# Optimization experiments

Measured on AMD Instinct MI355X. Metric: run time of the kernel, lower is better.

The kernel has to match this reference:

```python
import jax, jax.numpy as jnp
import numpy as np

NEG_SLOPE = 0.2
EPS = 0.0  # default eps, non-trainable buffer
N_NODES = 50000
N_EDGES = 400000
D = 512  # state_dim


def setup_inputs() -> dict:
    key = jax.random.key(0)
    ks = jax.random.split(key, 8)
    x = jax.random.normal(ks[0], (N_NODES, D), dtype=jnp.float32)
    row = jax.random.randint(ks[1], (N_EDGES,), 0, N_NODES)
    col = jax.random.randint(ks[2], (N_EDGES,), 0, N_NODES)
    # remove_self_loops: guarantee no self loops at data-gen time (static shapes)
    col = jnp.where(row == col, (col + 1) % N_NODES, col)
    edge_index = jnp.stack([row, col], axis=0)  # [2, E]
    condition = jax.random.normal(ks[3], (1, 256), dtype=jnp.float32)
    scale = 1.0 / np.sqrt(256.0)
    Wk = jax.random.normal(ks[4], (256, 2 * D), dtype=jnp.float32) * scale
    W1 = jax.random.normal(ks[5], (D, 2 * D), dtype=jnp.float32) / np.sqrt(D)
    b1 = jnp.zeros((2 * D,), dtype=jnp.float32)
    W2 = jax.random.normal(ks[6], (2 * D, D), dtype=jnp.float32) / np.sqrt(2 * D)
    b2 = jnp.zeros((D,), dtype=jnp.float32)
    return {"x": x, "edge_index": edge_index, "condition": condition,
            "Wk": Wk, "W1": W1, "b1": b1, "W2": W2, "b2": b2}


def reference(x, edge_index, condition, Wk, W1, b1, W2, b2):
    row, col = edge_index[0], edge_index[1]
    key = condition @ Wk                      # [1, 2D]
    ki, kj = key[0, :D], key[0, D:]           # x_i pairs with first half, x_j with second
    x_i = x[col]                              # [E, D]
    # alpha = (cat([x_i, x_j]) * key).sum(-1) without materializing the concat
    alpha = x_i @ ki + x[row] @ kj            # [E]
    alpha = jnp.where(alpha >= 0, alpha, NEG_SLOPE * alpha)  # leaky_relu
    alpha = jax.nn.sigmoid(alpha)
    agg = jax.ops.segment_sum(x_i * alpha[:, None], row, num_segments=x.shape[0])
    out = (1.0 + EPS) * x + agg
    out = jax.nn.relu(out @ W1 + b1) @ W2 + b2  # h_Theta MLP
    return out
```

## Files before the change

kernel.cpp:

```cpp
#include <hip/hip_runtime.h>

#define D 512
#define H1 1024
#define NNODES 50000
#define NEDGES 400000
#define MPAD 50048
#define NEG_SLOPE 0.2f
#define SCAN_BLOCKS 196

typedef __attribute__((ext_vector_type(8))) short bf16x8;
typedef __attribute__((ext_vector_type(8))) unsigned short u16x8;
typedef __attribute__((ext_vector_type(4))) float f32x4;


__device__ __forceinline__ unsigned short f2bf(float f) {
  unsigned int u = __float_as_uint(f);
  unsigned int r = u + 0x7FFFu + ((u >> 16) & 1u);
  return (unsigned short)(r >> 16);
}
__device__ __forceinline__ float bf2f(unsigned short h) {
  return __uint_as_float((unsigned int)h << 16);
}

__device__ __forceinline__ void gl_lds16(const void* g, void* l) {
  __builtin_amdgcn_global_load_lds(
      (const __attribute__((address_space(1))) void*)g,
      (__attribute__((address_space(3))) void*)l, 16, 0, 0);
}

__global__ void key_kernel(const float* __restrict__ cond, const float* __restrict__ Wk,
                           float* __restrict__ key) {
  int j = blockIdx.x * blockDim.x + threadIdx.x;
  if (j >= 2 * D) return;
  float s = 0.f;
#pragma unroll 8
  for (int i = 0; i < 256; ++i) s += cond[i] * Wk[i * (2 * D) + j];
  key[j] = s;
}

__global__ void nodedot_kernel(const float* __restrict__ x, const float* __restrict__ key,
                               float* __restrict__ nki, float* __restrict__ nkj,
                               unsigned short* __restrict__ xb) {
  int wid = (blockIdx.x * blockDim.x + threadIdx.x) >> 6;
  int lane = threadIdx.x & 63;
  if (wid >= NNODES) return;
  const float4* xr = (const float4*)(x + (size_t)wid * D);
  float4 p0 = xr[2 * lane], p1 = xr[2 * lane + 1];
  const float4* kia = (const float4*)key;
  const float4* kja = (const float4*)(key + D);
  float4 q0 = kia[2 * lane], q1 = kia[2 * lane + 1];
  float4 r0 = kja[2 * lane], r1 = kja[2 * lane + 1];
  float a = p0.x * q0.x + p0.y * q0.y + p0.z * q0.z + p0.w * q0.w +
            p1.x * q1.x + p1.y * q1.y + p1.z * q1.z + p1.w * q1.w;
  float b = p0.x * r0.x + p0.y * r0.y + p0.z * r0.z + p0.w * r0.w +
            p1.x * r1.x + p1.y * r1.y + p1.z * r1.z + p1.w * r1.w;
  u16x8 h;
  h[0] = f2bf(p0.x); h[1] = f2bf(p0.y); h[2] = f2bf(p0.z); h[3] = f2bf(p0.w);
  h[4] = f2bf(p1.x); h[5] = f2bf(p1.y); h[6] = f2bf(p1.z); h[7] = f2bf(p1.w);
  *(u16x8*)(xb + (size_t)wid * D + 8 * lane) = h;
#pragma unroll
  for (int off = 32; off > 0; off >>= 1) {
    a += __shfl_xor(a, off);
    b += __shfl_xor(b, off);
  }
  if (lane == 0) { nki[wid] = a; nkj[wid] = b; }
}

__global__ void convw_kernel(const float* __restrict__ W1, const float* __restrict__ W2,
                             unsigned short* __restrict__ W1t, unsigned short* __restrict__ W2t) {
  int idx = blockIdx.x * blockDim.x + threadIdx.x;
  if (idx >= D * H1) return;
  {
    int k = idx / H1, n = idx % H1;
    size_t a = (((size_t)(n >> 7) * (D >> 3) + (k >> 3)) << 10) + ((n & 127) << 3) + (k & 7);
    W1t[a] = f2bf(W1[idx]);
  }
  {
    int k = idx / D, n = idx % D;
    size_t a = (((size_t)(n >> 7) * (H1 >> 3) + (k >> 3)) << 10) + ((n & 127) << 3) + (k & 7);
    W2t[a] = f2bf(W2[idx]);
  }
}

__global__ void zero_deg_kernel(int* __restrict__ deg) {
  int i = blockIdx.x * blockDim.x + threadIdx.x;
  if (i < NNODES) deg[i] = 0;
}

__global__ void hist_kernel(const int* __restrict__ row, int* __restrict__ deg) {
  int e = blockIdx.x * blockDim.x + threadIdx.x;
  if (e < NEDGES) atomicAdd(&deg[row[e]], 1);
}

__global__ void scan1_kernel(const int* __restrict__ deg, int* __restrict__ rowptr,
                             int* __restrict__ blktot) {
  __shared__ int s[256];
  int tid = threadIdx.x;
  int i = blockIdx.x * 256 + tid;
  int v = (i < NNODES) ? deg[i] : 0;
  s[tid] = v;
  __syncthreads();
#pragma unroll
  for (int off = 1; off < 256; off <<= 1) {
    int t = (tid >= off) ? s[tid - off] : 0;
    __syncthreads();
    s[tid] += t;
    __syncthreads();
  }
  if (i < NNODES) rowptr[i] = s[tid] - v;
  if (tid == 255) blktot[blockIdx.x] = s[255];
}

__global__ void scan2_kernel(int* __restrict__ blktot, int* __restrict__ blkoff) {
  __shared__ int s[256];
  int tid = threadIdx.x;
  int v = (tid < SCAN_BLOCKS) ? blktot[tid] : 0;
  s[tid] = v;
  __syncthreads();
#pragma unroll
  for (int off = 1; off < 256; off <<= 1) {
    int t = (tid >= off) ? s[tid - off] : 0;
    __syncthreads();
    s[tid] += t;
    __syncthreads();
  }
  if (tid < SCAN_BLOCKS) blkoff[tid] = s[tid] - v;
}

__global__ void scan3_kernel(int* __restrict__ rowptr, const int* __restrict__ blkoff,
                             int* __restrict__ cursor) {
  int i = blockIdx.x * blockDim.x + threadIdx.x;
  if (i < NNODES) {
    int v = rowptr[i] + blkoff[blockIdx.x];
    rowptr[i] = v;
    cursor[i] = v;
  }
  if (i == 0) rowptr[NNODES] = NEDGES;
}

__global__ void fill_kernel(const int* __restrict__ row, const int* __restrict__ col,
                            const float* __restrict__ nki, const float* __restrict__ nkj,
                            int* __restrict__ cursor, int* __restrict__ scol,
                            float* __restrict__ salpha) {
  int e = blockIdx.x * blockDim.x + threadIdx.x;
  if (e >= NEDGES) return;
  int r = row[e], c = col[e];
  float a = nki[c] + nkj[r];
  a = (a >= 0.f) ? a : NEG_SLOPE * a;
  float al = 1.f / (1.f + expf(-a));
  int pos = atomicAdd(&cursor[r], 1);
  scol[pos] = c;
  salpha[pos] = al;
}

__global__ __launch_bounds__(256) void agg_kernel(
    const unsigned short* __restrict__ xb, const int* __restrict__ rowptr,
    const int* __restrict__ scol, const float* __restrict__ salpha,
    unsigned short* __restrict__ Pb) {
  int n = (blockIdx.x * blockDim.x + threadIdx.x) >> 6;
  int lane = threadIdx.x & 63;
  if (n >= NNODES) return;
  int beg = rowptr[n], end = rowptr[n + 1];
  u16x8 self = *(const u16x8*)(xb + (size_t)n * D + 8 * lane);
  float sa[8], sb[8];
#pragma unroll
  for (int q = 0; q < 8; ++q) { sa[q] = bf2f(self[q]); sb[q] = 0.f; }
  int e = beg;
  for (; e + 1 < end; e += 2) {
    int c0 = scol[e], c1 = scol[e + 1];
    float al0 = salpha[e], al1 = salpha[e + 1];
    u16x8 w0 = *(const u16x8*)(xb + (size_t)c0 * D + 8 * lane);
    u16x8 w1 = *(const u16x8*)(xb + (size_t)c1 * D + 8 * lane);
#pragma unroll
    for (int q = 0; q < 8; ++q) {
      sa[q] += al0 * bf2f(w0[q]);
      sb[q] += al1 * bf2f(w1[q]);
    }
  }
  if (e < end) {
    int c0 = scol[e];
    float al0 = salpha[e];
    u16x8 w0 = *(const u16x8*)(xb + (size_t)c0 * D + 8 * lane);
#pragma unroll
    for (int q = 0; q < 8; ++q) sa[q] += al0 * bf2f(w0[q]);
  }
  u16x8 h;
#pragma unroll
  for (int q = 0; q < 8; ++q) h[q] = f2bf(sa[q] + sb[q]);
  *(u16x8*)(Pb + (((size_t)(n >> 7) * (D >> 3) + lane) << 10) + ((n & 127) << 3)) = h;
}

template <bool RELU_OUT_BF16>
__global__ __launch_bounds__(256) void gemm_kernel(
    const unsigned short* __restrict__ Ag, const unsigned short* __restrict__ Bt,
    const float* __restrict__ bias, void* __restrict__ Cptr, int M_valid, int K, int N) {
  __shared__ unsigned short As[8 * 128 * 8];
  __shared__ unsigned short Bs[8 * 128 * 8];

  const int G = gridDim.x * gridDim.y;
  const int orig = blockIdx.y * gridDim.x + blockIdx.x;
  const int qq = G >> 3, rr = G & 7;
  const int xcd = orig & 7, loc = orig >> 3;
  const int wg = (xcd < rr ? xcd * (qq + 1) : rr * (qq + 1) + (xcd - rr) * qq) + loc;
  const int bx = wg % gridDim.x;
  const int by = wg / gridDim.x;

  const int tid = threadIdx.x;
  const int lane = tid & 63;
  const int wave = tid >> 6;
  const int wm = (wave >> 1) * 64;
  const int wn = (wave & 1) * 64;
  const int n0 = bx * 128;
  const int fr = lane & 15;
  const int kq = lane >> 4;

  const unsigned short* Apan = Ag + ((size_t)by * (K >> 3) << 10);
  const unsigned short* Bpan = Bt + ((size_t)bx * (K >> 3) << 10);

  f32x4 acc[4][4];
#pragma unroll
  for (int i = 0; i < 4; ++i)
#pragma unroll
    for (int j = 0; j < 4; ++j)
#pragma unroll
      for (int r = 0; r < 4; ++r) acc[i][j][r] = 0.f;

  for (int k0 = 0; k0 < K; k0 += 64) {
#pragma unroll
    for (int ss = 0; ss < 4; ++ss) {
      int s = wave * 4 + ss;
      int rbase = (s & 1) * 64;
      int kca = (k0 >> 3) + (s >> 1);
      gl_lds16(Apan + ((size_t)kca << 10) + (rbase + lane) * 8, &As[s * 512]);
      gl_lds16(Bpan + ((size_t)kca << 10) + (rbase + lane) * 8, &Bs[s * 512]);
    }
    __syncthreads();

#pragma unroll
    for (int h = 0; h < 2; ++h) {
      const int kc = h * 4 + kq;
      bf16x8 af[4], bfr[4];
#pragma unroll
      for (int i = 0; i < 4; ++i)
        af[i] = *(const bf16x8*)&As[(kc * 128 + wm + i * 16 + fr) * 8];
#pragma unroll
      for (int j = 0; j < 4; ++j)
        bfr[j] = *(const bf16x8*)&Bs[(kc * 128 + wn + j * 16 + fr) * 8];
#pragma unroll
      for (int i = 0; i < 4; ++i)
#pragma unroll
        for (int j = 0; j < 4; ++j)
          acc[i][j] = __builtin_amdgcn_mfma_f32_16x16x32_bf16(af[i], bfr[j], acc[i][j], 0, 0, 0);
    }
    __syncthreads();
  }

  const int rg = kq * 4;
#pragma unroll
  for (int i = 0; i < 4; ++i) {
#pragma unroll
    for (int j = 0; j < 4; ++j) {
      int gn = n0 + wn + j * 16 + fr;
      float bv = bias[gn];
#pragma unroll
      for (int r = 0; r < 4; ++r) {
        int lr = wm + i * 16 + rg + r;
        float v = acc[i][j][r] + bv;
        if constexpr (RELU_OUT_BF16) {
          v = fmaxf(v, 0.f);
          size_t a = (((size_t)by * (N >> 3) + (gn >> 3)) << 10) + (lr << 3) + (gn & 7);
          ((unsigned short*)Cptr)[a] = f2bf(v);
        } else {
          int gm = by * 128 + lr;
          if (gm < M_valid) ((float*)Cptr)[(size_t)gm * N + gn] = v;
        }
      }
    }
  }
}

extern "C" void kernel_launch(void* const* d_in, const int* in_sizes, int n_in,
                              void* d_out, int out_size, void* d_ws, size_t ws_size,
                              hipStream_t stream) {
  const float* x    = (const float*)d_in[0];
  const int*   ei   = (const int*)d_in[1];
  const float* cond = (const float*)d_in[2];
  const float* Wk   = (const float*)d_in[3];
  const float* W1   = (const float*)d_in[4];
  const float* b1   = (const float*)d_in[5];
  const float* W2   = (const float*)d_in[6];
  const float* b2   = (const float*)d_in[7];
  float* out = (float*)d_out;

  char* ws = (char*)d_ws;
  size_t off = 0;
  auto alloc = [&](size_t b) { size_t p = off; off += (b + 255) & ~(size_t)255; return p; };
  float* key = (float*)(ws + alloc(2 * D * sizeof(float)));
  float* nki = (float*)(ws + alloc(NNODES * sizeof(float)));
  float* nkj = (float*)(ws + alloc(NNODES * sizeof(float)));
  int* deg    = (int*)(ws + alloc(NNODES * sizeof(int)));
  int* rowptr = (int*)(ws + alloc((NNODES + 1) * sizeof(int)));
  int* cursor = (int*)(ws + alloc(NNODES * sizeof(int)));
  int* blktot = (int*)(ws + alloc(SCAN_BLOCKS * sizeof(int)));
  int* blkoff = (int*)(ws + alloc(SCAN_BLOCKS * sizeof(int)));
  int* scol      = (int*)(ws + alloc(NEDGES * sizeof(int)));
  float* salpha  = (float*)(ws + alloc(NEDGES * sizeof(float)));
  unsigned short* xb  = (unsigned short*)(ws + alloc((size_t)NNODES * D * 2));
  unsigned short* W1t = (unsigned short*)(ws + alloc((size_t)H1 * D * 2));
  unsigned short* W2t = (unsigned short*)(ws + alloc((size_t)D * H1 * 2));
  unsigned short* Pb  = (unsigned short*)(ws + alloc((size_t)MPAD * D * 2));
  unsigned short* Hb  = (unsigned short*)(ws + alloc((size_t)MPAD * H1 * 2));

  const int* row = ei;
  const int* col = ei + NEDGES;

  key_kernel<<<dim3((2 * D + 255) / 256), dim3(256), 0, stream>>>(cond, Wk, key);
  nodedot_kernel<<<dim3(NNODES * 64 / 256), dim3(256), 0, stream>>>(x, key, nki, nkj, xb);
  convw_kernel<<<dim3(D * H1 / 256), dim3(256), 0, stream>>>(W1, W2, W1t, W2t);

  zero_deg_kernel<<<dim3(SCAN_BLOCKS), dim3(256), 0, stream>>>(deg);
  hist_kernel<<<dim3((NEDGES + 255) / 256), dim3(256), 0, stream>>>(row, deg);
  scan1_kernel<<<dim3(SCAN_BLOCKS), dim3(256), 0, stream>>>(deg, rowptr, blktot);
  scan2_kernel<<<dim3(1), dim3(256), 0, stream>>>(blktot, blkoff);
  scan3_kernel<<<dim3(SCAN_BLOCKS), dim3(256), 0, stream>>>(rowptr, blkoff, cursor);
  fill_kernel<<<dim3((NEDGES + 255) / 256), dim3(256), 0, stream>>>(row, col, nki, nkj,
                                                                    cursor, scol, salpha);
  agg_kernel<<<dim3(NNODES * 64 / 256 + 1), dim3(256), 0, stream>>>(xb, rowptr, scol, salpha, Pb);

  gemm_kernel<true><<<dim3(H1 / 128, MPAD / 128), dim3(256), 0, stream>>>(
      Pb, W1t, b1, Hb, NNODES, D, H1);
  gemm_kernel<false><<<dim3(D / 128, MPAD / 128), dim3(256), 0, stream>>>(
      Hb, W2t, b2, out, NNODES, H1, D);
}
```

Before: 360.6 us.

## Use 256x256 double-buffered GEMM tiles with 8 waves and prefetch pipeline

Both MLP GEMMs now use 256x256 output tiles computed by 512-thread blocks (8 waves, each computing 128x64). Global-to-LDS loads are double-buffered two k-steps ahead, gated by explicit vmcnt waits and barriers, and MFMA sections run at raised wave priority. The aim is more data reuse per LDS load and overlap of memory traffic with MFMA work. The costs are more LDS (128 KB per block) and registers, fewer blocks in the grid, and padding M to 50176, which adds rows of wasted compute.

```diff
diff --git a/kernel.cpp b/kernel.cpp
--- a/kernel.cpp
+++ b/kernel.cpp
@@ -4,7 +4,7 @@
 #define H1 1024
 #define NNODES 50000
 #define NEDGES 400000
-#define MPAD 50048
+#define MPAD 50176
 #define NEG_SLOPE 0.2f
 #define SCAN_BLOCKS 196
 
@@ -190,88 +190,146 @@
   *(u16x8*)(Pb + (((size_t)(n >> 7) * (D >> 3) + lane) << 10) + ((n & 127) << 3)) = h;
 }
 
-template <bool RELU_OUT_BF16>
-__global__ __launch_bounds__(256) void gemm_kernel(
+template <int K, bool RELU_OUT_BF16>
+__global__ __launch_bounds__(512, 2) void gemm_kernel(
     const unsigned short* __restrict__ Ag, const unsigned short* __restrict__ Bt,
-    const float* __restrict__ bias, void* __restrict__ Cptr, int M_valid, int K, int N) {
-  __shared__ unsigned short As[8 * 128 * 8];
-  __shared__ unsigned short Bs[8 * 128 * 8];
+    const float* __restrict__ bias, void* __restrict__ Cptr, int M_valid, int N) {
+  constexpr int KC = K >> 3;
+  constexpr int NT = K >> 6;
+  __shared__ unsigned short As[2 * 2 * 8 * 128 * 8];
+  __shared__ unsigned short Bs[2 * 2 * 8 * 128 * 8];
 
   const int G = gridDim.x * gridDim.y;
   const int orig = blockIdx.y * gridDim.x + blockIdx.x;
-  const int qq = G >> 3, rr = G & 7;
-  const int xcd = orig & 7, loc = orig >> 3;
-  const int wg = (xcd < rr ? xcd * (qq + 1) : rr * (qq + 1) + (xcd - rr) * qq) + loc;
+  const int wg = (orig & 7) * (G >> 3) + (orig >> 3);
   const int bx = wg % gridDim.x;
   const int by = wg / gridDim.x;
 
   const int tid = threadIdx.x;
   const int lane = tid & 63;
   const int wave = tid >> 6;
-  const int wm = (wave >> 1) * 64;
-  const int wn = (wave & 1) * 64;
-  const int n0 = bx * 128;
+  const int wr = wave >> 2;
+  const int wc = wave & 3;
   const int fr = lane & 15;
   const int kq = lane >> 4;
 
-  const unsigned short* Apan = Ag + ((size_t)by * (K >> 3) << 10);
-  const unsigned short* Bpan = Bt + ((size_t)bx * (K >> 3) << 10);
-
-  f32x4 acc[4][4];
-#pragma unroll
-  for (int i = 0; i < 4; ++i)
+  f32x4 acc[8][4];
+#pragma unroll
+  for (int i = 0; i < 8; ++i)
 #pragma unroll
     for (int j = 0; j < 4; ++j)
 #pragma unroll
       for (int r = 0; r < 4; ++r) acc[i][j][r] = 0.f;
 
-  for (int k0 = 0; k0 < K; k0 += 64) {
+  auto stage = [&](int b, int t) {
 #pragma unroll
     for (int ss = 0; ss < 4; ++ss) {
-      int s = wave * 4 + ss;
-      int rbase = (s & 1) * 64;
-      int kca = (k0 >> 3) + (s >> 1);
-      gl_lds16(Apan + ((size_t)kca << 10) + (rbase + lane) * 8, &As[s * 512]);
-      gl_lds16(Bpan + ((size_t)kca << 10) + (rbase + lane) * 8, &Bs[s * 512]);
-    }
-    __syncthreads();
-
+      const int s = wave * 4 + ss;
+      const int rb = s >> 4, kc = (s >> 1) & 7, half = s & 1;
+      const int kca = t * 8 + kc;
+      gl_lds16(Ag + (((size_t)(by * 2 + rb) * KC + kca) << 10) + (half * 64 + lane) * 8,
+               &As[((b * 2 + rb) * 8 + kc) * 1024 + half * 512]);
+      gl_lds16(Bt + (((size_t)(bx * 2 + rb) * KC + kca) << 10) + (half * 64 + lane) * 8,
+               &Bs[((b * 2 + rb) * 8 + kc) * 1024 + half * 512]);
+    }
+  };
+
+  const int rbB = wc >> 1;
+  const int rowB = (wc & 1) * 64;
+
+  stage(0, 0);
+  stage(1, 1);
+
+  for (int t = 0; t < NT - 1; ++t) {
+    const int cur = t & 1;
+    asm volatile("s_waitcnt vmcnt(8)" ::: "memory");
+    __builtin_amdgcn_s_barrier();
+    __builtin_amdgcn_sched_barrier(0);
+
+    {
+      const int kc = kq;
+      bf16x8 af[8], bfv[4];
+#pragma unroll
+      for (int i = 0; i < 8; ++i)
+        af[i] = *(const bf16x8*)&As[((cur * 2 + wr) * 8 + kc) * 1024 + (i * 16 + fr) * 8];
+#pragma unroll
+      for (int j = 0; j < 4; ++j)
+        bfv[j] = *(const bf16x8*)&Bs[((cur * 2 + rbB) * 8 + kc) * 1024 + (rowB + j * 16 + fr) * 8];
+      __builtin_amdgcn_s_setprio(1);
+#pragma unroll
+      for (int i = 0; i < 8; ++i)
+#pragma unroll
+        for (int j = 0; j < 4; ++j)
+          acc[i][j] = __builtin_amdgcn_mfma_f32_16x16x32_bf16(af[i], bfv[j], acc[i][j], 0, 0, 0);
+      __builtin_amdgcn_s_setprio(0);
+    }
+
+    bf16x8 af1[8], bf1[4];
+    {
+      const int kc = 4 + kq;
+#pragma unroll
+      for (int i = 0; i < 8; ++i)
+        af1[i] = *(const bf16x8*)&As[((cur * 2 + wr) * 8 + kc) * 1024 + (i * 16 + fr) * 8];
+#pragma unroll
+      for (int j = 0; j < 4; ++j)
+        bf1[j] = *(const bf16x8*)&Bs[((cur * 2 + rbB) * 8 + kc) * 1024 + (rowB + j * 16 + fr) * 8];
+    }
+    asm volatile("s_waitcnt lgkmcnt(0)" ::: "memory");
+    __builtin_amdgcn_sched_barrier(0);
+    __builtin_amdgcn_s_barrier();
+    if (t + 2 < NT) stage(cur, t + 2);
+    __builtin_amdgcn_sched_barrier(0);
+    __builtin_amdgcn_s_setprio(1);
+#pragma unroll
+    for (int i = 0; i < 8; ++i)
+#pragma unroll
+      for (int j = 0; j < 4; ++j)
+        acc[i][j] = __builtin_amdgcn_mfma_f32_16x16x32_bf16(af1[i], bf1[j], acc[i][j], 0, 0, 0);
+    __builtin_amdgcn_s_setprio(0);
+  }
+
+  {
+    const int cur = (NT - 1) & 1;
+    asm volatile("s_waitcnt vmcnt(0)" ::: "memory");
+    __builtin_amdgcn_s_barrier();
+    __builtin_amdgcn_sched_barrier(0);
 #pragma unroll
     for (int h = 0; h < 2; ++h) {
       const int kc = h * 4 + kq;
-      bf16x8 af[4], bfr[4];
-#pragma unroll
-      for (int i = 0; i < 4; ++i)
-        af[i] = *(const bf16x8*)&As[(kc * 128 + wm + i * 16 + fr) * 8];
+      bf16x8 af[8], bfv[4];
+#pragma unroll
+      for (int i = 0; i < 8; ++i)
+        af[i] = *(const bf16x8*)&As[((cur * 2 + wr) * 8 + kc) * 1024 + (i * 16 + fr) * 8];
 #pragma unroll
       for (int j = 0; j < 4; ++j)
-        bfr[j] = *(const bf16x8*)&Bs[(kc * 128 + wn + j * 16 + fr) * 8];
-#pragma unroll
-      for (int i = 0; i < 4; ++i)
+        bfv[j] = *(const bf16x8*)&Bs[((cur * 2 + rbB) * 8 + kc) * 1024 + (rowB + j * 16 + fr) * 8];
+      __builtin_amdgcn_s_setprio(1);
+#pragma unroll
+      for (int i = 0; i < 8; ++i)
 #pragma unroll
         for (int j = 0; j < 4; ++j)
-          acc[i][j] = __builtin_amdgcn_mfma_f32_16x16x32_bf16(af[i], bfr[j], acc[i][j], 0, 0, 0);
-    }
-    __syncthreads();
+          acc[i][j] = __builtin_amdgcn_mfma_f32_16x16x32_bf16(af[i], bfv[j], acc[i][j], 0, 0, 0);
+      __builtin_amdgcn_s_setprio(0);
+    }
   }
 
   const int rg = kq * 4;
 #pragma unroll
-  for (int i = 0; i < 4; ++i) {
-#pragma unroll
-    for (int j = 0; j < 4; ++j) {
-      int gn = n0 + wn + j * 16 + fr;
-      float bv = bias[gn];
+  for (int j = 0; j < 4; ++j) {
+    const int gn = bx * 256 + wc * 64 + j * 16 + fr;
+    const float bv = bias[gn];
+#pragma unroll
+    for (int i = 0; i < 8; ++i) {
 #pragma unroll
       for (int r = 0; r < 4; ++r) {
-        int lr = wm + i * 16 + rg + r;
+        const int lrow = wr * 128 + i * 16 + rg + r;
+        const int gm = by * 256 + lrow;
         float v = acc[i][j][r] + bv;
         if constexpr (RELU_OUT_BF16) {
           v = fmaxf(v, 0.f);
-          size_t a = (((size_t)by * (N >> 3) + (gn >> 3)) << 10) + (lr << 3) + (gn & 7);
+          size_t a = (((size_t)(gm >> 7) * (N >> 3) + (gn >> 3)) << 10) + ((gm & 127) << 3) + (gn & 7);
           ((unsigned short*)Cptr)[a] = f2bf(v);
         } else {
-          int gm = by * 128 + lr;
           if (gm < M_valid) ((float*)Cptr)[(size_t)gm * N + gn] = v;
         }
       }
@@ -327,8 +385,8 @@
                                                                     cursor, scol, salpha);
   agg_kernel<<<dim3(NNODES * 64 / 256 + 1), dim3(256), 0, stream>>>(xb, rowptr, scol, salpha, Pb);
 
-  gemm_kernel<true><<<dim3(H1 / 128, MPAD / 128), dim3(256), 0, stream>>>(
-      Pb, W1t, b1, Hb, NNODES, D, H1);
-  gemm_kernel<false><<<dim3(D / 128, MPAD / 128), dim3(256), 0, stream>>>(
-      Hb, W2t, b2, out, NNODES, H1, D);
-}
+  gemm_kernel<512, true><<<dim3(H1 / 256, MPAD / 256), dim3(512), 0, stream>>>(
+      Pb, W1t, b1, Hb, NNODES, H1);
+  gemm_kernel<1024, false><<<dim3(D / 256, MPAD / 256), dim3(512), 0, stream>>>(
+      Hb, W2t, b2, out, NNODES, D);
+}
```

After: 371.3 us. 1.03x slower.

## Load GEMM fragments directly from global into registers with double buffering

Applied to the files above, without the earlier changes.

The GEMM kernels no longer stage A/B tiles through LDS with barriers. Each wave loads its MFMA fragments straight from the pre-tiled global layout into registers, using a two-set software pipeline with K as a template constant. MPAD grows so the block count divides evenly by 8, which lets the XCD remapping be simplified. This removes LDS traffic and syncthreads, but each wave now reads the tile data its neighbours also use, so reuse shifts from LDS to L2/L1 caches and global load traffic per block rises.

```diff
diff --git a/kernel.cpp b/kernel.cpp
--- a/kernel.cpp
+++ b/kernel.cpp
@@ -4,7 +4,7 @@
 #define H1 1024
 #define NNODES 50000
 #define NEDGES 400000
-#define MPAD 50048
+#define MPAD 50176
 #define NEG_SLOPE 0.2f
 #define SCAN_BLOCKS 196
 
@@ -20,12 +20,6 @@
 }
 __device__ __forceinline__ float bf2f(unsigned short h) {
   return __uint_as_float((unsigned int)h << 16);
-}
-
-__device__ __forceinline__ void gl_lds16(const void* g, void* l) {
-  __builtin_amdgcn_global_load_lds(
-      (const __attribute__((address_space(1))) void*)g,
-      (__attribute__((address_space(3))) void*)l, 16, 0, 0);
 }
 
 __global__ void key_kernel(const float* __restrict__ cond, const float* __restrict__ Wk,
@@ -190,32 +184,28 @@
   *(u16x8*)(Pb + (((size_t)(n >> 7) * (D >> 3) + lane) << 10) + ((n & 127) << 3)) = h;
 }
 
-template <bool RELU_OUT_BF16>
+template <int K, bool RELU_OUT_BF16>
 __global__ __launch_bounds__(256) void gemm_kernel(
     const unsigned short* __restrict__ Ag, const unsigned short* __restrict__ Bt,
-    const float* __restrict__ bias, void* __restrict__ Cptr, int M_valid, int K, int N) {
-  __shared__ unsigned short As[8 * 128 * 8];
-  __shared__ unsigned short Bs[8 * 128 * 8];
+    const float* __restrict__ bias, void* __restrict__ Cptr, int M_valid, int N) {
+  constexpr int KC = K >> 3;
+  constexpr int NSTEP = K >> 5;
 
   const int G = gridDim.x * gridDim.y;
   const int orig = blockIdx.y * gridDim.x + blockIdx.x;
-  const int qq = G >> 3, rr = G & 7;
-  const int xcd = orig & 7, loc = orig >> 3;
-  const int wg = (xcd < rr ? xcd * (qq + 1) : rr * (qq + 1) + (xcd - rr) * qq) + loc;
+  const int wg = (orig & 7) * (G >> 3) + (orig >> 3);
   const int bx = wg % gridDim.x;
   const int by = wg / gridDim.x;
 
-  const int tid = threadIdx.x;
-  const int lane = tid & 63;
-  const int wave = tid >> 6;
+  const int lane = threadIdx.x & 63;
+  const int wave = threadIdx.x >> 6;
   const int wm = (wave >> 1) * 64;
   const int wn = (wave & 1) * 64;
-  const int n0 = bx * 128;
   const int fr = lane & 15;
   const int kq = lane >> 4;
 
-  const unsigned short* Apan = Ag + ((size_t)by * (K >> 3) << 10);
-  const unsigned short* Bpan = Bt + ((size_t)bx * (K >> 3) << 10);
+  const unsigned short* Abase = Ag + (size_t)by * KC * 1024 + (wm + fr) * 8 + kq * 1024;
+  const unsigned short* Bbase = Bt + (size_t)bx * KC * 1024 + (wn + fr) * 8 + kq * 1024;
 
   f32x4 acc[4][4];
 #pragma unroll
@@ -225,53 +215,53 @@
 #pragma unroll
       for (int r = 0; r < 4; ++r) acc[i][j][r] = 0.f;
 
-  for (int k0 = 0; k0 < K; k0 += 64) {
-#pragma unroll
-    for (int ss = 0; ss < 4; ++ss) {
-      int s = wave * 4 + ss;
-      int rbase = (s & 1) * 64;
-      int kca = (k0 >> 3) + (s >> 1);
-      gl_lds16(Apan + ((size_t)kca << 10) + (rbase + lane) * 8, &As[s * 512]);
-      gl_lds16(Bpan + ((size_t)kca << 10) + (rbase + lane) * 8, &Bs[s * 512]);
-    }
-    __syncthreads();
-
-#pragma unroll
-    for (int h = 0; h < 2; ++h) {
-      const int kc = h * 4 + kq;
-      bf16x8 af[4], bfr[4];
-#pragma unroll
-      for (int i = 0; i < 4; ++i)
-        af[i] = *(const bf16x8*)&As[(kc * 128 + wm + i * 16 + fr) * 8];
-#pragma unroll
-      for (int j = 0; j < 4; ++j)
-        bfr[j] = *(const bf16x8*)&Bs[(kc * 128 + wn + j * 16 + fr) * 8];
-#pragma unroll
-      for (int i = 0; i < 4; ++i)
-#pragma unroll
-        for (int j = 0; j < 4; ++j)
-          acc[i][j] = __builtin_amdgcn_mfma_f32_16x16x32_bf16(af[i], bfr[j], acc[i][j], 0, 0, 0);
-    }
-    __syncthreads();
-  }
+  bf16x8 a0[4], b0[4], a1[4], b1[4];
+
+#define LOADSET(AV, BV, T)                                                 \
+  {                                                                        \
+    const unsigned short* ap_ = Abase + (size_t)(T) * 4096;                \
+    const unsigned short* bp_ = Bbase + (size_t)(T) * 4096;                \
+    _Pragma("unroll") for (int i = 0; i < 4; ++i)                          \
+        AV[i] = *(const bf16x8*)(ap_ + i * 128);                           \
+    _Pragma("unroll") for (int j = 0; j < 4; ++j)                          \
+        BV[j] = *(const bf16x8*)(bp_ + j * 128);                           \
+  }
+#define MFMASET(AV, BV)                                                    \
+  _Pragma("unroll") for (int i = 0; i < 4; ++i)                            \
+      _Pragma("unroll") for (int j = 0; j < 4; ++j)                        \
+          acc[i][j] = __builtin_amdgcn_mfma_f32_16x16x32_bf16(             \
+              AV[i], BV[j], acc[i][j], 0, 0, 0);
+
+  LOADSET(a0, b0, 0)
+  for (int t = 0; t < NSTEP - 2; t += 2) {
+    LOADSET(a1, b1, t + 1)
+    MFMASET(a0, b0)
+    LOADSET(a0, b0, t + 2)
+    MFMASET(a1, b1)
+  }
+  LOADSET(a1, b1, NSTEP - 1)
+  MFMASET(a0, b0)
+  MFMASET(a1, b1)
+#undef LOADSET
+#undef MFMASET
 
   const int rg = kq * 4;
 #pragma unroll
-  for (int i = 0; i < 4; ++i) {
-#pragma unroll
-    for (int j = 0; j < 4; ++j) {
-      int gn = n0 + wn + j * 16 + fr;
-      float bv = bias[gn];
+  for (int j = 0; j < 4; ++j) {
+    const int gn = bx * 128 + wn + j * 16 + fr;
+    const float bv = bias[gn];
+#pragma unroll
+    for (int i = 0; i < 4; ++i) {
 #pragma unroll
       for (int r = 0; r < 4; ++r) {
-        int lr = wm + i * 16 + rg + r;
+        const int lrow = wm + i * 16 + rg + r;
+        const int gm = by * 128 + lrow;
         float v = acc[i][j][r] + bv;
         if constexpr (RELU_OUT_BF16) {
           v = fmaxf(v, 0.f);
-          size_t a = (((size_t)by * (N >> 3) + (gn >> 3)) << 10) + (lr << 3) + (gn & 7);
+          size_t a = (((size_t)by * (N >> 3) + (gn >> 3)) << 10) + (lrow << 3) + (gn & 7);
           ((unsigned short*)Cptr)[a] = f2bf(v);
         } else {
-          int gm = by * 128 + lr;
           if (gm < M_valid) ((float*)Cptr)[(size_t)gm * N + gn] = v;
         }
       }
@@ -327,8 +317,8 @@
                                                                     cursor, scol, salpha);
   agg_kernel<<<dim3(NNODES * 64 / 256 + 1), dim3(256), 0, stream>>>(xb, rowptr, scol, salpha, Pb);
 
-  gemm_kernel<true><<<dim3(H1 / 128, MPAD / 128), dim3(256), 0, stream>>>(
-      Pb, W1t, b1, Hb, NNODES, D, H1);
-  gemm_kernel<false><<<dim3(D / 128, MPAD / 128), dim3(256), 0, stream>>>(
-      Hb, W2t, b2, out, NNODES, H1, D);
-}
+  gemm_kernel<512, true><<<dim3(H1 / 128, MPAD / 128), dim3(256), 0, stream>>>(
+      Pb, W1t, b1, Hb, NNODES, H1);
+  gemm_kernel<1024, false><<<dim3(D / 128, MPAD / 128), dim3(256), 0, stream>>>(
+      Hb, W2t, b2, out, NNODES, D);
+}
```

New measurement: 394.7 us. 9.5% more time.

## Replace GEMMs with 256x256-tile 8-wave double-buffered pipelined MFMA kernel

Applied to the files above, without the earlier changes.

Both MLP GEMMs move from a 128x128 tile kernel with 4 waves and a single LDS buffer to a 256x256 tile kernel with 8 waves. The new kernel double-buffers LDS, interleaves global-to-LDS staging with MFMA phases under explicit vmcnt/lgkmcnt waits, and raises wave priority around MFMA bursts. The goal is to hide load latency and get more reuse per LDS byte. It needs M padded to 50176 and much more LDS per block, and it removes the uneven-split handling in the XCD remap (which is exact only when the block count divides by 8).

```diff
diff --git a/kernel.cpp b/kernel.cpp
--- a/kernel.cpp
+++ b/kernel.cpp
@@ -4,7 +4,7 @@
 #define H1 1024
 #define NNODES 50000
 #define NEDGES 400000
-#define MPAD 50048
+#define MPAD 50176
 #define NEG_SLOPE 0.2f
 #define SCAN_BLOCKS 196
 
@@ -190,88 +190,144 @@
   *(u16x8*)(Pb + (((size_t)(n >> 7) * (D >> 3) + lane) << 10) + ((n & 127) << 3)) = h;
 }
 
-template <bool RELU_OUT_BF16>
-__global__ __launch_bounds__(256) void gemm_kernel(
+template <int K, bool RELU_OUT_BF16>
+__global__ __launch_bounds__(512, 2) void gemm8p(
     const unsigned short* __restrict__ Ag, const unsigned short* __restrict__ Bt,
-    const float* __restrict__ bias, void* __restrict__ Cptr, int M_valid, int K, int N) {
-  __shared__ unsigned short As[8 * 128 * 8];
-  __shared__ unsigned short Bs[8 * 128 * 8];
+    const float* __restrict__ bias, void* __restrict__ Cptr, int M_valid, int N) {
+  constexpr int KC = K >> 3;
+  constexpr int NT = K >> 6;
+  __shared__ unsigned short As[2 * 2 * 8 * 1024];
+  __shared__ unsigned short Bs[2 * 2 * 8 * 1024];
 
   const int G = gridDim.x * gridDim.y;
   const int orig = blockIdx.y * gridDim.x + blockIdx.x;
-  const int qq = G >> 3, rr = G & 7;
-  const int xcd = orig & 7, loc = orig >> 3;
-  const int wg = (xcd < rr ? xcd * (qq + 1) : rr * (qq + 1) + (xcd - rr) * qq) + loc;
+  const int wg = (orig & 7) * (G >> 3) + (orig >> 3);
   const int bx = wg % gridDim.x;
   const int by = wg / gridDim.x;
 
   const int tid = threadIdx.x;
   const int lane = tid & 63;
   const int wave = tid >> 6;
-  const int wm = (wave >> 1) * 64;
-  const int wn = (wave & 1) * 64;
-  const int n0 = bx * 128;
+  const int wr = wave >> 2;
+  const int wc = wave & 3;
   const int fr = lane & 15;
   const int kq = lane >> 4;
-
-  const unsigned short* Apan = Ag + ((size_t)by * (K >> 3) << 10);
-  const unsigned short* Bpan = Bt + ((size_t)bx * (K >> 3) << 10);
-
-  f32x4 acc[4][4];
-#pragma unroll
-  for (int i = 0; i < 4; ++i)
-#pragma unroll
-    for (int j = 0; j < 4; ++j)
-#pragma unroll
-      for (int r = 0; r < 4; ++r) acc[i][j][r] = 0.f;
-
-  for (int k0 = 0; k0 < K; k0 += 64) {
-#pragma unroll
-    for (int ss = 0; ss < 4; ++ss) {
-      int s = wave * 4 + ss;
-      int rbase = (s & 1) * 64;
-      int kca = (k0 >> 3) + (s >> 1);
-      gl_lds16(Apan + ((size_t)kca << 10) + (rbase + lane) * 8, &As[s * 512]);
-      gl_lds16(Bpan + ((size_t)kca << 10) + (rbase + lane) * 8, &Bs[s * 512]);
+  const int bh = wc >> 1;
+  const int bc0 = (wc & 1) * 64;
+
+  f32x4 acc[8][4];
+#pragma unroll
+  for (int m = 0; m < 8; ++m)
+#pragma unroll
+    for (int n = 0; n < 4; ++n)
+#pragma unroll
+      for (int r = 0; r < 4; ++r) acc[m][n][r] = 0.f;
+
+  bf16x8 aR[2][4];
+  bf16x8 bC[2][2][2];
+
+  auto stage = [&](const unsigned short* __restrict__ Gp, int bcoord, int buf, int h,
+                   int t, unsigned short* Ls) {
+#pragma unroll
+    for (int L = 0; L < 2; ++L) {
+      const int g = L * 512 + tid;
+      const int kc = g >> 7, rw = g & 127;
+      gl_lds16(Gp + (((size_t)(bcoord * 2 + h) * KC + t * 8 + kc) << 10) + rw * 8,
+               Ls + (((buf * 2 + h) * 8 + kc) << 10) + rw * 8);
     }
-    __syncthreads();
-
-#pragma unroll
-    for (int h = 0; h < 2; ++h) {
-      const int kc = h * 4 + kq;
-      bf16x8 af[4], bfr[4];
+  };
+  auto dsA = [&](int buf, int rh) {
+#pragma unroll
+    for (int ks = 0; ks < 2; ++ks)
 #pragma unroll
       for (int i = 0; i < 4; ++i)
-        af[i] = *(const bf16x8*)&As[(kc * 128 + wm + i * 16 + fr) * 8];
-#pragma unroll
-      for (int j = 0; j < 4; ++j)
-        bfr[j] = *(const bf16x8*)&Bs[(kc * 128 + wn + j * 16 + fr) * 8];
+        aR[ks][i] = *(const bf16x8*)&As[(((buf * 2 + wr) * 8 + ks * 4 + kq) << 10) +
+                                        (rh * 64 + i * 16 + fr) * 8];
+  };
+  auto dsB = [&](int buf, int ch) {
+#pragma unroll
+    for (int ks = 0; ks < 2; ++ks)
+#pragma unroll
+      for (int j = 0; j < 2; ++j)
+        bC[ch][ks][j] = *(const bf16x8*)&Bs[(((buf * 2 + bh) * 8 + ks * 4 + kq) << 10) +
+                                            (bc0 + ch * 32 + j * 16 + fr) * 8];
+  };
+  auto mfma16 = [&](int rh, int ch) {
+#pragma unroll
+    for (int ks = 0; ks < 2; ++ks)
 #pragma unroll
       for (int i = 0; i < 4; ++i)
 #pragma unroll
-        for (int j = 0; j < 4; ++j)
-          acc[i][j] = __builtin_amdgcn_mfma_f32_16x16x32_bf16(af[i], bfr[j], acc[i][j], 0, 0, 0);
-    }
-    __syncthreads();
-  }
+        for (int j = 0; j < 2; ++j)
+          acc[rh * 4 + i][ch * 2 + j] = __builtin_amdgcn_mfma_f32_16x16x32_bf16(
+              aR[ks][i], bC[ch][ks][j], acc[rh * 4 + i][ch * 2 + j], 0, 0, 0);
+  };
+
+#define LGKM0 asm volatile("s_waitcnt lgkmcnt(0)" ::: "memory"); \
+              __builtin_amdgcn_sched_barrier(0)
+#define PRIO1 __builtin_amdgcn_s_setprio(1)
+#define PRIO0 __builtin_amdgcn_s_setprio(0)
+#define BAR   __builtin_amdgcn_s_barrier()
+
+  stage(Ag, by, 0, 0, 0, As); stage(Ag, by, 0, 1, 0, As);
+  stage(Bt, bx, 0, 0, 0, Bs); stage(Bt, bx, 0, 1, 0, Bs);
+  stage(Bt, bx, 1, 0, 1, Bs); stage(Bt, bx, 1, 1, 1, Bs);
+
+  for (int it = 0; it < NT / 2; ++it) {
+    const int t0 = 2 * it;
+    const bool more = (t0 + 2 < NT);
+    const bool more3 = (t0 + 3 < NT);
+    stage(Ag, by, 1, 0, t0 + 1, As);
+    asm volatile("s_waitcnt vmcnt(6)" ::: "memory");
+    BAR;
+    dsA(0, 0); dsB(0, 0);
+    LGKM0; PRIO1; mfma16(0, 0); PRIO0; BAR;
+    dsB(0, 1);
+    stage(Ag, by, 1, 1, t0 + 1, As);
+    LGKM0; PRIO1; mfma16(0, 1); PRIO0; BAR;
+    dsA(0, 1);
+    if (more) stage(Bt, bx, 0, 0, t0 + 2, Bs);
+    LGKM0; PRIO1; mfma16(1, 0); PRIO0; BAR;
+    if (more) stage(Bt, bx, 0, 1, t0 + 2, Bs);
+    PRIO1; mfma16(1, 1); PRIO0; BAR;
+    if (more) stage(Ag, by, 0, 0, t0 + 2, As);
+    if (more) { asm volatile("s_waitcnt vmcnt(6)" ::: "memory"); }
+    else      { asm volatile("s_waitcnt vmcnt(0)" ::: "memory"); }
+    BAR;
+    dsA(1, 0); dsB(1, 0);
+    LGKM0; PRIO1; mfma16(0, 0); PRIO0; BAR;
+    dsB(1, 1);
+    if (more) stage(Ag, by, 0, 1, t0 + 2, As);
+    LGKM0; PRIO1; mfma16(0, 1); PRIO0; BAR;
+    dsA(1, 1);
+    if (more3) stage(Bt, bx, 1, 0, t0 + 3, Bs);
+    LGKM0; PRIO1; mfma16(1, 0); PRIO0; BAR;
+    if (more3) stage(Bt, bx, 1, 1, t0 + 3, Bs);
+    PRIO1; mfma16(1, 1); PRIO0; BAR;
+  }
+#undef LGKM0
+#undef PRIO1
+#undef PRIO0
+#undef BAR
 
   const int rg = kq * 4;
 #pragma unroll
-  for (int i = 0; i < 4; ++i) {
-#pragma unroll
-    for (int j = 0; j < 4; ++j) {
-      int gn = n0 + wn + j * 16 + fr;
-      float bv = bias[gn];
+  for (int n = 0; n < 4; ++n) {
+    const int gn = bx * 256 + wc * 64 + (n >> 1) * 32 + (n & 1) * 16 + fr;
+    const float bvl = bias[gn];
+#pragma unroll
+    for (int m = 0; m < 8; ++m) {
 #pragma unroll
       for (int r = 0; r < 4; ++r) {
-        int lr = wm + i * 16 + rg + r;
-        float v = acc[i][j][r] + bv;
+        const int lrow = wr * 128 + (m >> 2) * 64 + (m & 3) * 16 + rg + r;
+        const int gm = by * 256 + lrow;
+        float v = acc[m][n][r] + bvl;
         if constexpr (RELU_OUT_BF16) {
           v = fmaxf(v, 0.f);
-          size_t a = (((size_t)by * (N >> 3) + (gn >> 3)) << 10) + (lr << 3) + (gn & 7);
+          size_t a = (((size_t)(gm >> 7) * (N >> 3) + (gn >> 3)) << 10) +
+                     ((gm & 127) << 3) + (gn & 7);
           ((unsigned short*)Cptr)[a] = f2bf(v);
         } else {
-          int gm = by * 128 + lr;
           if (gm < M_valid) ((float*)Cptr)[(size_t)gm * N + gn] = v;
         }
       }
@@ -327,8 +383,8 @@
                                                                     cursor, scol, salpha);
   agg_kernel<<<dim3(NNODES * 64 / 256 + 1), dim3(256), 0, stream>>>(xb, rowptr, scol, salpha, Pb);
 
-  gemm_kernel<true><<<dim3(H1 / 128, MPAD / 128), dim3(256), 0, stream>>>(
-      Pb, W1t, b1, Hb, NNODES, D, H1);
-  gemm_kernel<false><<<dim3(D / 128, MPAD / 128), dim3(256), 0, stream>>>(
-      Hb, W2t, b2, out, NNODES, H1, D);
-}
+  gemm8p<512, true><<<dim3(H1 / 256, MPAD / 256), dim3(512), 0, stream>>>(
+      Pb, W1t, b1, Hb, NNODES, H1);
+  gemm8p<1024, false><<<dim3(D / 256, MPAD / 256), dim3(512), 0, stream>>>(
+      Hb, W2t, b2, out, NNODES, D);
+}
```

Result: slower. 397.5 us (+10.2%).
